# Kernel optimization log

Measured on AMD Instinct MI355X. Metric: run time of the kernel, lower is better.

## Reference

```python
import jax, jax.numpy as jnp
import numpy as np

# surrogate-gradient spike (multi-gaussian, standard DH-SNN act_fun_adp constants)
GAMMA, LENS, SCALE, HIGHT = 0.5, 0.5, 6.0, 0.15
B_J0, BETA_ADAPT, VTH = 1.6, 1.8, 1.0
IN_DIM, N1, N2, OUT_DIM, BRANCH = 76, 50, 100, 2, 4
BATCH, SEQ = 256, 1000

def _gauss(x, mu, sigma):
    return jnp.exp(-((x - mu) ** 2) / (2.0 * sigma ** 2)) / (jnp.sqrt(2.0 * jnp.pi) * sigma)

@jax.custom_vjp
def spike_fn(x):
    return (x > 0).astype(x.dtype)

def _spike_fwd(x):
    return spike_fn(x), x

def _spike_bwd(x, g):
    sg = (_gauss(x, 0.0, LENS) * (1.0 + HIGHT)
          - _gauss(x, LENS, SCALE * LENS) * HIGHT
          - _gauss(x, -LENS, SCALE * LENS) * HIGHT)
    return (g * sg * GAMMA,)

spike_fn.defvjp(_spike_fwd, _spike_bwd)

def branch_mask(in_dim, out_dim, branch):
    # each dendritic branch k sees contiguous chunk k of the (input|recurrent) vector
    isize = in_dim + out_dim
    seg = int(np.ceil(isize / branch))
    m = np.zeros((out_dim * branch, isize), np.float32)
    for k in range(branch):
        m[k::branch, k * seg:min((k + 1) * seg, isize)] = 1.0
    return jnp.asarray(m)

def setup_inputs():
    key = jax.random.key(0)
    ks = jax.random.split(key, 12)
    def lin(k, o, i):
        lim = 1.0 / np.sqrt(i)
        kw, kb = jax.random.split(k)
        return (jax.random.uniform(kw, (o, i), jnp.float32, -lim, lim),
                jax.random.uniform(kb, (o,), jnp.float32, -lim, lim))
    W1, b1 = lin(ks[0], N1 * BRANCH, IN_DIM + N1)
    W2, b2 = lin(ks[1], N2 * BRANCH, N1 + N2)
    Wx, bx = lin(ks[2], N2, 2 * N2)
    Wm, bm = lin(ks[3], N2, 2 * N2)
    Wa, ba = lin(ks[4], N2, 2 * N2)
    Wd = jax.random.normal(ks[5], (OUT_DIM, N2), jnp.float32) * np.sqrt(2.0 / (OUT_DIM + N2))
    bd = jnp.zeros((OUT_DIM,), jnp.float32)
    tau_m1 = jax.random.uniform(ks[6], (N1,), jnp.float32, 0.0, 4.0)
    tau_n1 = jax.random.uniform(ks[7], (N1, BRANCH), jnp.float32, 0.0, 4.0)
    tau_m2 = jax.random.uniform(ks[8], (N2,), jnp.float32, 0.0, 4.0)
    tau_n2 = jax.random.uniform(ks[9], (N2, BRANCH), jnp.float32, 0.0, 4.0)
    tau_md = jax.random.uniform(ks[10], (OUT_DIM,), jnp.float32, 0.0, 4.0)
    x = jax.random.normal(ks[11], (BATCH, SEQ, IN_DIM), jnp.float32)
    return dict(x=x, W1=W1, b1=b1, tau_m1=tau_m1, tau_n1=tau_n1,
                W2=W2, b2=b2, tau_m2=tau_m2, tau_n2=tau_n2,
                Wx=Wx, bx=bx, Wm=Wm, bm=bm, Wa=Wa, ba=ba,
                Wd=Wd, bd=bd, tau_md=tau_md)

def _denri_step(xt, mem, spk, d, W, b, tau_m, tau_n, n_out):
    # dendritic spiking neuron (spike_rnn_test_denri_wotanh_R)
    kin = jnp.concatenate([xt, spk], axis=1)                       # [B, in+out]
    beta = jax.nn.sigmoid(tau_n)                                   # [out, branch]
    proj = (kin @ W.T + b).reshape(-1, n_out, BRANCH)              # [B, out, branch]
    d = beta * d + (1.0 - beta) * proj
    alpha = jax.nn.sigmoid(tau_m)
    mem = mem * alpha + (1.0 - alpha) * d.sum(-1) - VTH * spk
    spk = spike_fn(mem - VTH)
    return mem, spk, d

def _liquid_step(xt, mem, spk, bth, Wx, bx, Wm, bm, Wa, ba):
    # liquid time-constant adaptive-threshold cell (SNN_rec_cell, is_rec=True)
    dx = jnp.concatenate([xt, spk], axis=1) @ Wx.T + bx
    tauM = jax.nn.sigmoid(jnp.concatenate([dx, mem], axis=1) @ Wm.T + bm)
    tauA = jax.nn.sigmoid(jnp.concatenate([dx, bth], axis=1) @ Wa.T + ba)
    bth = tauA * bth + (1.0 - tauA) * spk
    B = B_J0 + BETA_ADAPT * bth
    mem = mem * tauM + (1.0 - tauM) * dx - B * spk
    spk = spike_fn(mem - B)
    return mem, spk, bth

def reference(x, W1, b1, tau_m1, tau_n1, W2, b2, tau_m2, tau_n2,
              Wx, bx, Wm, bm, Wa, ba, Wd, bd, tau_md):
    Bsz = x.shape[0]
    W1m = W1 * branch_mask(IN_DIM, N1, BRANCH)
    W2m = W2 * branch_mask(N1, N2, BRANCH)
    alpha_d = jax.nn.sigmoid(tau_md)
    z = lambda *s: jnp.zeros(s, x.dtype)
    carry0 = (z(Bsz, N1), z(Bsz, N1), z(Bsz, N1, BRANCH),
              z(Bsz, N2), z(Bsz, N2), z(Bsz, N2, BRANCH),
              z(Bsz, N2), z(Bsz, N2), jnp.full((Bsz, N2), B_J0, x.dtype),
              z(Bsz, OUT_DIM))

    def step(carry, xt):
        m1, s1, d1, m2, s2, d2, lm, ls, lb, md = carry
        m1, s1, d1 = _denri_step(xt, m1, s1, d1, W1m, b1, tau_m1, tau_n1, N1)
        m2, s2, d2 = _denri_step(s1, m2, s2, d2, W2m, b2, tau_m2, tau_n2, N2)
        # original detaches the liquid hidden tuple every step
        lm, ls, lb = (jax.lax.stop_gradient(t) for t in (lm, ls, lb))
        lm, ls, lb = _liquid_step(s2, lm, ls, lb, Wx, bx, Wm, bm, Wa, ba)
        md = md * alpha_d + (1.0 - alpha_d) * (ls @ Wd.T + bd)    # readout integrator
        return (m1, s1, d1, m2, s2, d2, lm, ls, lb, md), md

    _, md_seq = jax.lax.scan(step, carry0, jnp.swapaxes(x, 0, 1))  # [T, B, OUT]
    return md_seq[1:].sum(axis=0)  # output only accumulated for i > 0
```

## Files before the change

kernel.cpp:

```cpp
#include <hip/hip_runtime.h>
#include <math.h>

#define SEQ 1000
#define IND 76
#define PIDX(i) ((((i)/25)*28) + ((i)%25))

__device__ __forceinline__ float sigf(float v) { return 1.0f / (1.0f + expf(-v)); }

__global__ __launch_bounds__(512) void dhsnn_fwd(
    const float* __restrict__ x,
    const float* __restrict__ W1, const float* __restrict__ b1,
    const float* __restrict__ tau_m1, const float* __restrict__ tau_n1,
    const float* __restrict__ W2, const float* __restrict__ b2,
    const float* __restrict__ tau_m2, const float* __restrict__ tau_n2,
    const float* __restrict__ Wxp, const float* __restrict__ bxp,
    const float* __restrict__ Wm, const float* __restrict__ bm,
    const float* __restrict__ Wa, const float* __restrict__ ba,
    const float* __restrict__ Wd, const float* __restrict__ bd,
    const float* __restrict__ tau_md,
    float* __restrict__ out)
{
    const int t   = (int)threadIdx.x;
    const int blk = (int)blockIdx.x;

    __shared__ __align__(16) float kin1P[128];
    __shared__ __align__(16) float kin2P[4][40];
    __shared__ __align__(16) float s1stage[56];
    __shared__ __align__(16) float dsum[400];
    __shared__ __align__(16) float dpart[8][100];
    __shared__ __align__(16) float spart[8][200];
    __shared__ __align__(16) float dxP[112];
    __shared__ __align__(16) float s2P[112];
    __shared__ __align__(16) float lsP[112];
    __shared__ __align__(16) float lmP[112];
    __shared__ __align__(16) float lbP[112];
    __shared__ __align__(16) float tauA_s[100];
    __shared__ __align__(16) float rpart[200];
    __shared__ __align__(16) float r2[8];

    for (int i = t; i < 128;  i += 512) kin1P[i] = 0.f;
    for (int i = t; i < 160;  i += 512) (&kin2P[0][0])[i] = 0.f;
    for (int i = t; i < 56;   i += 512) s1stage[i] = 0.f;
    for (int i = t; i < 400;  i += 512) dsum[i] = 0.f;
    for (int i = t; i < 800;  i += 512) (&dpart[0][0])[i] = 0.f;
    for (int i = t; i < 1600; i += 512) (&spart[0][0])[i] = 0.f;
    for (int i = t; i < 112;  i += 512) { dxP[i]=0.f; s2P[i]=0.f; lsP[i]=0.f; lmP[i]=0.f; lbP[i]=0.f; }
    for (int i = t; i < 100;  i += 512) tauA_s[i] = 0.f;
    for (int i = t; i < 200;  i += 512) rpart[i] = 0.f;
    for (int i = t; i < 8;    i += 512) r2[i] = 0.f;

    float wreg[188];
    float sc[10];
    float st[8];
    float mdr = 0.f, accr = 0.f;
    float4 xp0;
    #pragma unroll
    for (int i = 0; i < 10; ++i) sc[i] = 0.f;
    #pragma unroll
    for (int i = 0; i < 8; ++i)  st[i] = 0.f;

    if (t < 456) {
        const bool late = (t >= 256);
        const int  s    = late ? (t - 256) : t;
        if (s < 200) {
            const int g = s >> 2, c = s & 3;
            const int colbase = late ? (25 * c) : (100 + 25 * c);
            #pragma unroll
            for (int k = 0; k < 4; ++k) {
                const int row = 4 * g + k;
                const float* Wrow = (row < 100) ? (Wm + row * 200) : (Wa + (row - 100) * 200);
                #pragma unroll
                for (int u = 0; u < 25; ++u) wreg[k * 25 + u] = Wrow[colbase + u];
            }
            #pragma unroll
            for (int k = 0; k < 2; ++k) {
                const int row = 2 * g + k;
                #pragma unroll
                for (int u = 0; u < 25; ++u) wreg[100 + k * 25 + u] = Wxp[row * 200 + colbase + u];
            }
        }
        if (t < 400) {
            const int br = t & 3;
            #pragma unroll
            for (int cc = 0; cc < 38; ++cc) {
                const int gc = 38 * br + cc;
                wreg[150 + cc] = (gc < 150) ? W2[t * 150 + gc] : 0.f;
            }
            sc[0] = b2[t];
            sc[1] = sigf(tau_n2[t]);
        }
        if (t < 200) sc[5] = Wd[(t < 100 ? 0 : 100) + (t % 100)];
        if (t < 100) { sc[2] = sigf(tau_m2[t]); sc[3] = bxp[t]; sc[4] = bm[t]; st[3] = 1.6f; }
        else if (t < 200) sc[4] = ba[t - 100];
        if (t < 2) { sc[6] = sigf(tau_md[t]); sc[7] = bd[t]; }
    } else if (t < 506) {
        const int n = t - 456;
        #pragma unroll
        for (int k = 0; k < 4; ++k) {
            #pragma unroll
            for (int u = 0; u < 32; ++u) {
                const int gc = 32 * k + u;
                wreg[k * 32 + u] = (gc < 126) ? W1[(4 * n + k) * 126 + gc] : 0.f;
            }
            sc[k]     = b1[4 * n + k];
            sc[4 + k] = sigf(tau_n1[4 * n + k]);
        }
        sc[8] = sigf(tau_m1[n]);
    }

    auto l1_step = [&]() {
        float pr0 = sc[0], pr1 = sc[1], pr2 = sc[2], pr3 = sc[3];
        #pragma unroll
        for (int u4 = 0; u4 < 8; ++u4) {
            const float4 a0 = *reinterpret_cast<const float4*>(&kin1P[ 0 + 4 * u4]);
            const float4 a1 = *reinterpret_cast<const float4*>(&kin1P[32 + 4 * u4]);
            const float4 a2 = *reinterpret_cast<const float4*>(&kin1P[64 + 4 * u4]);
            const float4 a3 = *reinterpret_cast<const float4*>(&kin1P[96 + 4 * u4]);
            pr0 = fmaf(wreg[      4*u4+0], a0.x, pr0); pr0 = fmaf(wreg[      4*u4+1], a0.y, pr0);
            pr0 = fmaf(wreg[      4*u4+2], a0.z, pr0); pr0 = fmaf(wreg[      4*u4+3], a0.w, pr0);
            pr1 = fmaf(wreg[ 32 + 4*u4+0], a1.x, pr1); pr1 = fmaf(wreg[ 32 + 4*u4+1], a1.y, pr1);
            pr1 = fmaf(wreg[ 32 + 4*u4+2], a1.z, pr1); pr1 = fmaf(wreg[ 32 + 4*u4+3], a1.w, pr1);
            pr2 = fmaf(wreg[ 64 + 4*u4+0], a2.x, pr2); pr2 = fmaf(wreg[ 64 + 4*u4+1], a2.y, pr2);
            pr2 = fmaf(wreg[ 64 + 4*u4+2], a2.z, pr2); pr2 = fmaf(wreg[ 64 + 4*u4+3], a2.w, pr2);
            pr3 = fmaf(wreg[ 96 + 4*u4+0], a3.x, pr3); pr3 = fmaf(wreg[ 96 + 4*u4+1], a3.y, pr3);
            pr3 = fmaf(wreg[ 96 + 4*u4+2], a3.z, pr3); pr3 = fmaf(wreg[ 96 + 4*u4+3], a3.w, pr3);
        }
        const float d0 = sc[4] * st[0] + (1.f - sc[4]) * pr0;
        const float d1 = sc[5] * st[1] + (1.f - sc[5]) * pr1;
        const float d2 = sc[6] * st[2] + (1.f - sc[6]) * pr2;
        const float d3 = sc[7] * st[3] + (1.f - sc[7]) * pr3;
        st[0] = d0; st[1] = d1; st[2] = d2; st[3] = d3;
        const float sum = ((d0 + d1) + d2) + d3;
        st[4] = sc[8] * st[4] + (1.f - sc[8]) * sum - st[5];
        st[5] = (st[4] - 1.0f > 0.f) ? 1.f : 0.f;
        s1stage[t - 456] = st[5];
    };

    __syncthreads();
    if (t < 100) lbP[PIDX(t)] = 1.6f;
    if (t < 19) {
        const float4 v = *reinterpret_cast<const float4*>(x + (size_t)blk * SEQ * IND + 4 * t);
        *reinterpret_cast<float4*>(&kin1P[4 * t]) = v;
    }
    __syncthreads();
    if (t >= 456 && t < 506) l1_step();
    __syncthreads();
    if (t >= 128 && t < 178) {
        const int i2 = t - 128;
        const float v = s1stage[i2];
        kin1P[76 + i2] = v;
        const int w = i2 / 38;
        kin2P[w][i2 - 38 * w] = v;
    }
    if (t < 19) {
        const float4 v = *reinterpret_cast<const float4*>(x + ((size_t)blk * SEQ + 1) * IND + 4 * t);
        *reinterpret_cast<float4*>(&kin1P[4 * t]) = v;
    }
    __syncthreads();

    for (int j = 0; j < SEQ; ++j) {
        if (t >= 456) {
            if (t < 506 && j < SEQ - 1) l1_step();
        } else {
            if (t < 400) {
                const float* kw = kin2P[t & 3];
                float a0 = 0.f, a1 = 0.f, a2 = 0.f, a3 = 0.f;
                #pragma unroll
                for (int cc = 0; cc < 9; ++cc) {
                    const float4 av = *reinterpret_cast<const float4*>(kw + 4 * cc);
                    a0 = fmaf(wreg[150 + 4*cc + 0], av.x, a0);
                    a1 = fmaf(wreg[150 + 4*cc + 1], av.y, a1);
                    a2 = fmaf(wreg[150 + 4*cc + 2], av.z, a2);
                    a3 = fmaf(wreg[150 + 4*cc + 3], av.w, a3);
                }
                a0 = fmaf(wreg[186], kw[36], a0);
                a1 = fmaf(wreg[187], kw[37], a1);
                const float proj = sc[0] + ((a0 + a1) + (a2 + a3));
                st[0] = sc[1] * st[0] + (1.f - sc[1]) * proj;
                dsum[t] = st[0];
            }
            if (t < 200) {
                const int g = t >> 2, c = t & 3;
                {
                    const float* ap = ((g < 25) ? lmP : lbP) + 28 * c;
                    float e0=0.f, e1=0.f, e2=0.f, e3=0.f;
                    #pragma unroll
                    for (int u4 = 0; u4 < 6; ++u4) {
                        const float4 av = *reinterpret_cast<const float4*>(ap + 4 * u4);
                        e0 = fmaf(wreg[  0 + 4*u4+0], av.x, e0); e0 = fmaf(wreg[  0 + 4*u4+1], av.y, e0);
                        e0 = fmaf(wreg[  0 + 4*u4+2], av.z, e0); e0 = fmaf(wreg[  0 + 4*u4+3], av.w, e0);
                        e1 = fmaf(wreg[ 25 + 4*u4+0], av.x, e1); e1 = fmaf(wreg[ 25 + 4*u4+1], av.y, e1);
                        e1 = fmaf(wreg[ 25 + 4*u4+2], av.z, e1); e1 = fmaf(wreg[ 25 + 4*u4+3], av.w, e1);
                        e2 = fmaf(wreg[ 50 + 4*u4+0], av.x, e2); e2 = fmaf(wreg[ 50 + 4*u4+1], av.y, e2);
                        e2 = fmaf(wreg[ 50 + 4*u4+2], av.z, e2); e2 = fmaf(wreg[ 50 + 4*u4+3], av.w, e2);
                        e3 = fmaf(wreg[ 75 + 4*u4+0], av.x, e3); e3 = fmaf(wreg[ 75 + 4*u4+1], av.y, e3);
                        e3 = fmaf(wreg[ 75 + 4*u4+2], av.z, e3); e3 = fmaf(wreg[ 75 + 4*u4+3], av.w, e3);
                    }
                    const float al = ap[24];
                    e0 = fmaf(wreg[24], al, e0); e1 = fmaf(wreg[49], al, e1);
                    e2 = fmaf(wreg[74], al, e2); e3 = fmaf(wreg[99], al, e3);
                    spart[c][4*g+0] = e0; spart[c][4*g+1] = e1;
                    spart[c][4*g+2] = e2; spart[c][4*g+3] = e3;
                }
                {
                    const float* ap = lsP + 28 * c;
                    float f0 = 0.f, f1 = 0.f;
                    #pragma unroll
                    for (int u4 = 0; u4 < 6; ++u4) {
                        const float4 av = *reinterpret_cast<const float4*>(ap + 4 * u4);
                        f0 = fmaf(wreg[100 + 4*u4+0], av.x, f0); f0 = fmaf(wreg[100 + 4*u4+1], av.y, f0);
                        f0 = fmaf(wreg[100 + 4*u4+2], av.z, f0); f0 = fmaf(wreg[100 + 4*u4+3], av.w, f0);
                        f1 = fmaf(wreg[125 + 4*u4+0], av.x, f1); f1 = fmaf(wreg[125 + 4*u4+1], av.y, f1);
                        f1 = fmaf(wreg[125 + 4*u4+2], av.z, f1); f1 = fmaf(wreg[125 + 4*u4+3], av.w, f1);
                    }
                    const float al = ap[24];
                    f0 = fmaf(wreg[124], al, f0);
                    f1 = fmaf(wreg[149], al, f1);
                    dpart[c][2*g+0] = f0;
                    dpart[c][2*g+1] = f1;
                }
                rpart[t] = sc[5] * lsP[PIDX(t % 100)];
            } else if (t < 219) {
                if (j + 2 < SEQ)
                    xp0 = *reinterpret_cast<const float4*>(x + ((size_t)blk * SEQ + (j + 2)) * IND + 4 * (t - 200));
            }
        }
        __syncthreads();
        if (t < 100) {
            const float4 dv = *reinterpret_cast<const float4*>(&dsum[4 * t]);
            const float sum = ((dv.x + dv.y) + dv.z) + dv.w;
            st[1] = sc[2] * st[1] + (1.f - sc[2]) * sum - st[7];
            st[7] = (st[1] - 1.0f > 0.f) ? 1.f : 0.f;
            const int col = 50 + t, w = col / 38;
            kin2P[w][col - 38 * w] = st[7];
            s2P[PIDX(t)] = st[7];
        } else if (t >= 256 && t < 264) {
            const int rr = t - 256;
            float sV = 0.f;
            #pragma unroll
            for (int u = 0; u < 25; ++u) sV += rpart[25 * rr + u];
            r2[rr] = sV;
        }
        __syncthreads();
        if (t >= 256 && t < 456) {
            const int s = t - 256;
            const int g = s >> 2, c = s & 3;
            const float* ap = s2P + 28 * c;
            float f0 = 0.f, f1 = 0.f;
            #pragma unroll
            for (int u4 = 0; u4 < 6; ++u4) {
                const float4 av = *reinterpret_cast<const float4*>(ap + 4 * u4);
                f0 = fmaf(wreg[100 + 4*u4+0], av.x, f0); f0 = fmaf(wreg[100 + 4*u4+1], av.y, f0);
                f0 = fmaf(wreg[100 + 4*u4+2], av.z, f0); f0 = fmaf(wreg[100 + 4*u4+3], av.w, f0);
                f1 = fmaf(wreg[125 + 4*u4+0], av.x, f1); f1 = fmaf(wreg[125 + 4*u4+1], av.y, f1);
                f1 = fmaf(wreg[125 + 4*u4+2], av.z, f1); f1 = fmaf(wreg[125 + 4*u4+3], av.w, f1);
            }
            const float al = ap[24];
            f0 = fmaf(wreg[124], al, f0);
            f1 = fmaf(wreg[149], al, f1);
            dpart[4 + c][2*g+0] = f0;
            dpart[4 + c][2*g+1] = f1;
        } else if (t >= 200 && t < 219) {
            if (j + 2 < SEQ)
                *reinterpret_cast<float4*>(&kin1P[4 * (t - 200)]) = xp0;
        }
        __syncthreads();
        if (t < 100) {
            const float sV = (((dpart[4][t] + dpart[5][t]) + (dpart[6][t] + dpart[7][t]))
                            + ((dpart[0][t] + dpart[1][t]) + (dpart[2][t] + dpart[3][t]))) + sc[3];
            st[5] = sV;
            dxP[PIDX(t)] = sV;
        }
        if (t < 2 && j >= 1) {
            const float dot = ((r2[4*t+0] + r2[4*t+1]) + (r2[4*t+2] + r2[4*t+3])) + sc[7];
            mdr = sc[6] * mdr + (1.f - sc[6]) * dot;
            if (j >= 2) accr += mdr;
        }
        __syncthreads();
        if (t >= 256 && t < 456) {
            const int s = t - 256;
            const int g = s >> 2, c = s & 3;
            const float* ap = dxP + 28 * c;
            float e0=0.f, e1=0.f, e2=0.f, e3=0.f;
            #pragma unroll
            for (int u4 = 0; u4 < 6; ++u4) {
                const float4 av = *reinterpret_cast<const float4*>(ap + 4 * u4);
                e0 = fmaf(wreg[  0 + 4*u4+0], av.x, e0); e0 = fmaf(wreg[  0 + 4*u4+1], av.y, e0);
                e0 = fmaf(wreg[  0 + 4*u4+2], av.z, e0); e0 = fmaf(wreg[  0 + 4*u4+3], av.w, e0);
                e1 = fmaf(wreg[ 25 + 4*u4+0], av.x, e1); e1 = fmaf(wreg[ 25 + 4*u4+1], av.y, e1);
                e1 = fmaf(wreg[ 25 + 4*u4+2], av.z, e1); e1 = fmaf(wreg[ 25 + 4*u4+3], av.w, e1);
                e2 = fmaf(wreg[ 50 + 4*u4+0], av.x, e2); e2 = fmaf(wreg[ 50 + 4*u4+1], av.y, e2);
                e2 = fmaf(wreg[ 50 + 4*u4+2], av.z, e2); e2 = fmaf(wreg[ 50 + 4*u4+3], av.w, e2);
                e3 = fmaf(wreg[ 75 + 4*u4+0], av.x, e3); e3 = fmaf(wreg[ 75 + 4*u4+1], av.y, e3);
                e3 = fmaf(wreg[ 75 + 4*u4+2], av.z, e3); e3 = fmaf(wreg[ 75 + 4*u4+3], av.w, e3);
            }
            const float al = ap[24];
            e0 = fmaf(wreg[24], al, e0); e1 = fmaf(wreg[49], al, e1);
            e2 = fmaf(wreg[74], al, e2); e3 = fmaf(wreg[99], al, e3);
            spart[4 + c][4*g+0] = e0; spart[4 + c][4*g+1] = e1;
            spart[4 + c][4*g+2] = e2; spart[4 + c][4*g+3] = e3;
        }
        __syncthreads();
        if (t < 200) {
            const float sV = (((spart[4][t] + spart[5][t]) + (spart[6][t] + spart[7][t]))
                            + ((spart[0][t] + spart[1][t]) + (spart[2][t] + spart[3][t]))) + sc[4];
            const float tv = 1.f / (1.f + expf(-sV));
            if (t < 100) st[6] = tv;
            else tauA_s[t - 100] = tv;
        }
        __syncthreads();
        if (t < 100) {
            const float ta  = tauA_s[t];
            const float lbN = ta * st[3] + (1.f - ta) * st[4];
            const float Bv  = 1.6f + 1.8f * lbN;
            const float lmN = st[2] * st[6] + (1.f - st[6]) * st[5] - Bv * st[4];
            const float lsN = (lmN - Bv > 0.f) ? 1.f : 0.f;
            st[2] = lmN; st[3] = lbN; st[4] = lsN;
            lmP[PIDX(t)] = lmN; lbP[PIDX(t)] = lbN; lsP[PIDX(t)] = lsN;
        } else if (t >= 128 && t < 178) {
            const int i2 = t - 128;
            const float v = s1stage[i2];
            kin1P[76 + i2] = v;
            const int w = i2 / 38;
            kin2P[w][i2 - 38 * w] = v;
        }
        __syncthreads();
    }

    if (t < 200) rpart[t] = sc[5] * lsP[PIDX(t % 100)];
    __syncthreads();
    if (t >= 256 && t < 264) {
        const int rr = t - 256;
        float sV = 0.f;
        #pragma unroll
        for (int u = 0; u < 25; ++u) sV += rpart[25 * rr + u];
        r2[rr] = sV;
    }
    __syncthreads();
    if (t < 2) {
        const float dot = ((r2[4*t+0] + r2[4*t+1]) + (r2[4*t+2] + r2[4*t+3])) + sc[7];
        mdr = sc[6] * mdr + (1.f - sc[6]) * dot;
        accr += mdr;
        out[blk * 2 + t] = accr;
    }
}

extern "C" void kernel_launch(void* const* d_in, const int* in_sizes, int n_in,
                              void* d_out, int out_size, void* d_ws, size_t ws_size,
                              hipStream_t stream) {
    const float* x      = (const float*)d_in[0];
    const float* W1     = (const float*)d_in[1];
    const float* b1     = (const float*)d_in[2];
    const float* tau_m1 = (const float*)d_in[3];
    const float* tau_n1 = (const float*)d_in[4];
    const float* W2     = (const float*)d_in[5];
    const float* b2     = (const float*)d_in[6];
    const float* tau_m2 = (const float*)d_in[7];
    const float* tau_n2 = (const float*)d_in[8];
    const float* Wx     = (const float*)d_in[9];
    const float* bx     = (const float*)d_in[10];
    const float* bm     = (const float*)d_in[12];
    const float* Wm     = (const float*)d_in[11];
    const float* Wa     = (const float*)d_in[13];
    const float* ba     = (const float*)d_in[14];
    const float* Wd     = (const float*)d_in[15];
    const float* bd     = (const float*)d_in[16];
    const float* tau_md = (const float*)d_in[17];
    float* out = (float*)d_out;

    const int batch = in_sizes[0] / (SEQ * IND);
    dhsnn_fwd<<<batch, 512, 0, stream>>>(x, W1, b1, tau_m1, tau_n1,
                                         W2, b2, tau_m2, tau_n2,
                                         Wx, bx, Wm, bm, Wa, ba,
                                         Wd, bd, tau_md, out);
}
```

Baseline: 4.654 ms.

## Restructure per-step work split to cut barriers using wave shuffles

Reassigns the 400 layer-2 threads so each group of four lanes owns one neuron, computing dendritic sums and the liquid-layer matvecs over half or quarter slices and combining partial sums with intra-wave shuffles. This replaces shared-memory partial arrays (dsum, dpart, spart, tauA_s) and cuts the barriers per timestep from six to three. It also sets launch bounds to two blocks per CU. The cost is a larger per-thread register array, more redundant work per lane, and possible spilling under the tighter register budget.

```diff
diff --git a/kernel.cpp b/kernel.cpp
--- a/kernel.cpp
+++ b/kernel.cpp
@@ -3,11 +3,16 @@
 
 #define SEQ 1000
 #define IND 76
-#define PIDX(i) ((((i)/25)*28) + ((i)%25))
 
 __device__ __forceinline__ float sigf(float v) { return 1.0f / (1.0f + expf(-v)); }
 
-__global__ __launch_bounds__(512) void dhsnn_fwd(
+#define W2O 0
+#define SEO 38
+#define SLO 90
+#define XEO 142
+#define XLO 170
+
+__global__ __launch_bounds__(512, 2) void dhsnn_fwd(
     const float* __restrict__ x,
     const float* __restrict__ W1, const float* __restrict__ b1,
     const float* __restrict__ tau_m1, const float* __restrict__ tau_n1,
@@ -26,75 +31,72 @@
     __shared__ __align__(16) float kin1P[128];
     __shared__ __align__(16) float kin2P[4][40];
     __shared__ __align__(16) float s1stage[56];
-    __shared__ __align__(16) float dsum[400];
-    __shared__ __align__(16) float dpart[8][100];
-    __shared__ __align__(16) float spart[8][200];
-    __shared__ __align__(16) float dxP[112];
-    __shared__ __align__(16) float s2P[112];
-    __shared__ __align__(16) float lsP[112];
-    __shared__ __align__(16) float lmP[112];
-    __shared__ __align__(16) float lbP[112];
-    __shared__ __align__(16) float tauA_s[100];
+    __shared__ __align__(16) float s2P[104];
+    __shared__ __align__(16) float dxP[104];
+    __shared__ __align__(16) float lsP[104];
+    __shared__ __align__(16) float lmP[104];
+    __shared__ __align__(16) float lbP[104];
     __shared__ __align__(16) float rpart[200];
     __shared__ __align__(16) float r2[8];
 
-    for (int i = t; i < 128;  i += 512) kin1P[i] = 0.f;
-    for (int i = t; i < 160;  i += 512) (&kin2P[0][0])[i] = 0.f;
-    for (int i = t; i < 56;   i += 512) s1stage[i] = 0.f;
-    for (int i = t; i < 400;  i += 512) dsum[i] = 0.f;
-    for (int i = t; i < 800;  i += 512) (&dpart[0][0])[i] = 0.f;
-    for (int i = t; i < 1600; i += 512) (&spart[0][0])[i] = 0.f;
-    for (int i = t; i < 112;  i += 512) { dxP[i]=0.f; s2P[i]=0.f; lsP[i]=0.f; lmP[i]=0.f; lbP[i]=0.f; }
-    for (int i = t; i < 100;  i += 512) tauA_s[i] = 0.f;
-    for (int i = t; i < 200;  i += 512) rpart[i] = 0.f;
-    for (int i = t; i < 8;    i += 512) r2[i] = 0.f;
-
-    float wreg[188];
-    float sc[10];
-    float st[8];
+    for (int i = t; i < 128; i += 512) kin1P[i] = 0.f;
+    for (int i = t; i < 160; i += 512) (&kin2P[0][0])[i] = 0.f;
+    for (int i = t; i < 56;  i += 512) s1stage[i] = 0.f;
+    for (int i = t; i < 104; i += 512) { s2P[i]=0.f; dxP[i]=0.f; lsP[i]=0.f; lmP[i]=0.f; lbP[i]=0.f; }
+    for (int i = t; i < 200; i += 512) rpart[i] = 0.f;
+    for (int i = t; i < 8;   i += 512) r2[i] = 0.f;
+
+    const int q = t >> 2;
+    const int c = t & 3;
+    const int h = c & 1;
+    const int lbase = (t & 63) & ~3;
+
+    float wreg[198];
+    float sc[9];
+    float st[7];
+    float eAcc = 0.f, dAcc = 0.f;
     float mdr = 0.f, accr = 0.f;
     float4 xp0;
+    int doff = 0;
     #pragma unroll
-    for (int i = 0; i < 10; ++i) sc[i] = 0.f;
+    for (int i = 0; i < 9; ++i) sc[i] = 0.f;
     #pragma unroll
-    for (int i = 0; i < 8; ++i)  st[i] = 0.f;
-
-    if (t < 456) {
-        const bool late = (t >= 256);
-        const int  s    = late ? (t - 256) : t;
-        if (s < 200) {
-            const int g = s >> 2, c = s & 3;
-            const int colbase = late ? (25 * c) : (100 + 25 * c);
-            #pragma unroll
-            for (int k = 0; k < 4; ++k) {
-                const int row = 4 * g + k;
-                const float* Wrow = (row < 100) ? (Wm + row * 200) : (Wa + (row - 100) * 200);
-                #pragma unroll
-                for (int u = 0; u < 25; ++u) wreg[k * 25 + u] = Wrow[colbase + u];
-            }
-            #pragma unroll
-            for (int k = 0; k < 2; ++k) {
-                const int row = 2 * g + k;
-                #pragma unroll
-                for (int u = 0; u < 25; ++u) wreg[100 + k * 25 + u] = Wxp[row * 200 + colbase + u];
-            }
-        }
-        if (t < 400) {
-            const int br = t & 3;
-            #pragma unroll
-            for (int cc = 0; cc < 38; ++cc) {
-                const int gc = 38 * br + cc;
-                wreg[150 + cc] = (gc < 150) ? W2[t * 150 + gc] : 0.f;
-            }
-            sc[0] = b2[t];
-            sc[1] = sigf(tau_n2[t]);
-        }
-        if (t < 200) sc[5] = Wd[(t < 100 ? 0 : 100) + (t % 100)];
-        if (t < 100) { sc[2] = sigf(tau_m2[t]); sc[3] = bxp[t]; sc[4] = bm[t]; st[3] = 1.6f; }
-        else if (t < 200) sc[4] = ba[t - 100];
-        if (t < 2) { sc[6] = sigf(tau_md[t]); sc[7] = bd[t]; }
-    } else if (t < 506) {
-        const int n = t - 456;
+    for (int i = 0; i < 7; ++i) st[i] = 0.f;
+
+    if (t < 400) {
+        #pragma unroll
+        for (int cc = 0; cc < 38; ++cc) {
+            const int gc = 38 * c + cc;
+            wreg[W2O + cc] = (gc < 150) ? W2[t * 150 + gc] : 0.f;
+        }
+        sc[0] = b2[t];
+        sc[1] = sigf(tau_n2[t]);
+        const float* Wrow = (c < 2) ? (Wm + q * 200) : (Wa + q * 200);
+        const int eoff = h ? 52 : 0;
+        #pragma unroll
+        for (int u = 0; u < 52; ++u) {
+            const int col = eoff + u;
+            const bool ok = (col < 100);
+            wreg[SEO + u] = ok ? Wrow[100 + col] : 0.f;
+            wreg[SLO + u] = ok ? Wrow[col] : 0.f;
+        }
+        doff = (c == 0) ? 0 : (4 + 24 * c);
+        const int dcnt = (c == 0) ? 28 : 24;
+        #pragma unroll
+        for (int u = 0; u < 28; ++u) {
+            const int col = doff + u;
+            const bool ok = (u < dcnt);
+            wreg[XEO + u] = ok ? Wxp[q * 200 + 100 + col] : 0.f;
+            wreg[XLO + u] = ok ? Wxp[q * 200 + col] : 0.f;
+        }
+        if (c == 0) {
+            sc[2] = sigf(tau_m2[q]);
+            sc[3] = bm[q]; sc[4] = ba[q]; sc[5] = bxp[q];
+            st[4] = 1.6f;
+        }
+        if (t < 200) sc[6] = Wd[(t < 100 ? 0 : 100) + (t % 100)];
+    } else if (t >= 448 && t < 498) {
+        const int n = t - 448;
         #pragma unroll
         for (int k = 0; k < 4; ++k) {
             #pragma unroll
@@ -106,6 +108,9 @@
             sc[4 + k] = sigf(tau_n1[4 * n + k]);
         }
         sc[8] = sigf(tau_m1[n]);
+    } else if (t == 420 || t == 421) {
+        sc[0] = sigf(tau_md[t - 420]);
+        sc[1] = bd[t - 420];
     }
 
     auto l1_step = [&]() {
@@ -133,17 +138,17 @@
         const float sum = ((d0 + d1) + d2) + d3;
         st[4] = sc[8] * st[4] + (1.f - sc[8]) * sum - st[5];
         st[5] = (st[4] - 1.0f > 0.f) ? 1.f : 0.f;
-        s1stage[t - 456] = st[5];
+        s1stage[t - 448] = st[5];
     };
 
     __syncthreads();
-    if (t < 100) lbP[PIDX(t)] = 1.6f;
+    if (t < 100) lbP[t] = 1.6f;
     if (t < 19) {
         const float4 v = *reinterpret_cast<const float4*>(x + (size_t)blk * SEQ * IND + 4 * t);
         *reinterpret_cast<float4*>(&kin1P[4 * t]) = v;
     }
     __syncthreads();
-    if (t >= 456 && t < 506) l1_step();
+    if (t >= 448 && t < 498) l1_step();
     __syncthreads();
     if (t >= 128 && t < 178) {
         const int i2 = t - 128;
@@ -159,189 +164,161 @@
     __syncthreads();
 
     for (int j = 0; j < SEQ; ++j) {
-        if (t >= 456) {
-            if (t < 506 && j < SEQ - 1) l1_step();
-        } else {
-            if (t < 400) {
-                const float* kw = kin2P[t & 3];
+        if (t < 400) {
+            {
+                const float* kw = kin2P[c];
                 float a0 = 0.f, a1 = 0.f, a2 = 0.f, a3 = 0.f;
                 #pragma unroll
                 for (int cc = 0; cc < 9; ++cc) {
                     const float4 av = *reinterpret_cast<const float4*>(kw + 4 * cc);
-                    a0 = fmaf(wreg[150 + 4*cc + 0], av.x, a0);
-                    a1 = fmaf(wreg[150 + 4*cc + 1], av.y, a1);
-                    a2 = fmaf(wreg[150 + 4*cc + 2], av.z, a2);
-                    a3 = fmaf(wreg[150 + 4*cc + 3], av.w, a3);
+                    a0 = fmaf(wreg[W2O + 4*cc + 0], av.x, a0);
+                    a1 = fmaf(wreg[W2O + 4*cc + 1], av.y, a1);
+                    a2 = fmaf(wreg[W2O + 4*cc + 2], av.z, a2);
+                    a3 = fmaf(wreg[W2O + 4*cc + 3], av.w, a3);
                 }
-                a0 = fmaf(wreg[186], kw[36], a0);
-                a1 = fmaf(wreg[187], kw[37], a1);
+                a0 = fmaf(wreg[W2O + 36], kw[36], a0);
+                a1 = fmaf(wreg[W2O + 37], kw[37], a1);
                 const float proj = sc[0] + ((a0 + a1) + (a2 + a3));
                 st[0] = sc[1] * st[0] + (1.f - sc[1]) * proj;
-                dsum[t] = st[0];
-            }
-            if (t < 200) {
-                const int g = t >> 2, c = t & 3;
-                {
-                    const float* ap = ((g < 25) ? lmP : lbP) + 28 * c;
-                    float e0=0.f, e1=0.f, e2=0.f, e3=0.f;
-                    #pragma unroll
-                    for (int u4 = 0; u4 < 6; ++u4) {
-                        const float4 av = *reinterpret_cast<const float4*>(ap + 4 * u4);
-                        e0 = fmaf(wreg[  0 + 4*u4+0], av.x, e0); e0 = fmaf(wreg[  0 + 4*u4+1], av.y, e0);
-                        e0 = fmaf(wreg[  0 + 4*u4+2], av.z, e0); e0 = fmaf(wreg[  0 + 4*u4+3], av.w, e0);
-                        e1 = fmaf(wreg[ 25 + 4*u4+0], av.x, e1); e1 = fmaf(wreg[ 25 + 4*u4+1], av.y, e1);
-                        e1 = fmaf(wreg[ 25 + 4*u4+2], av.z, e1); e1 = fmaf(wreg[ 25 + 4*u4+3], av.w, e1);
-                        e2 = fmaf(wreg[ 50 + 4*u4+0], av.x, e2); e2 = fmaf(wreg[ 50 + 4*u4+1], av.y, e2);
-                        e2 = fmaf(wreg[ 50 + 4*u4+2], av.z, e2); e2 = fmaf(wreg[ 50 + 4*u4+3], av.w, e2);
-                        e3 = fmaf(wreg[ 75 + 4*u4+0], av.x, e3); e3 = fmaf(wreg[ 75 + 4*u4+1], av.y, e3);
-                        e3 = fmaf(wreg[ 75 + 4*u4+2], av.z, e3); e3 = fmaf(wreg[ 75 + 4*u4+3], av.w, e3);
-                    }
-                    const float al = ap[24];
-                    e0 = fmaf(wreg[24], al, e0); e1 = fmaf(wreg[49], al, e1);
-                    e2 = fmaf(wreg[74], al, e2); e3 = fmaf(wreg[99], al, e3);
-                    spart[c][4*g+0] = e0; spart[c][4*g+1] = e1;
-                    spart[c][4*g+2] = e2; spart[c][4*g+3] = e3;
+                const float dme = st[0];
+                const float dd1 = __shfl(dme, lbase + 1, 64);
+                const float dd2 = __shfl(dme, lbase + 2, 64);
+                const float dd3 = __shfl(dme, lbase + 3, 64);
+                if (c == 0) {
+                    const float sum = ((dme + dd1) + dd2) + dd3;
+                    st[1] = sc[2] * st[1] + (1.f - sc[2]) * sum - st[2];
+                    st[2] = (st[1] - 1.0f > 0.f) ? 1.f : 0.f;
+                    s2P[q] = st[2];
                 }
-                {
-                    const float* ap = lsP + 28 * c;
-                    float f0 = 0.f, f1 = 0.f;
-                    #pragma unroll
-                    for (int u4 = 0; u4 < 6; ++u4) {
-                        const float4 av = *reinterpret_cast<const float4*>(ap + 4 * u4);
-                        f0 = fmaf(wreg[100 + 4*u4+0], av.x, f0); f0 = fmaf(wreg[100 + 4*u4+1], av.y, f0);
-                        f0 = fmaf(wreg[100 + 4*u4+2], av.z, f0); f0 = fmaf(wreg[100 + 4*u4+3], av.w, f0);
-                        f1 = fmaf(wreg[125 + 4*u4+0], av.x, f1); f1 = fmaf(wreg[125 + 4*u4+1], av.y, f1);
-                        f1 = fmaf(wreg[125 + 4*u4+2], av.z, f1); f1 = fmaf(wreg[125 + 4*u4+3], av.w, f1);
-                    }
-                    const float al = ap[24];
-                    f0 = fmaf(wreg[124], al, f0);
-                    f1 = fmaf(wreg[149], al, f1);
-                    dpart[c][2*g+0] = f0;
-                    dpart[c][2*g+1] = f1;
+            }
+            {
+                const float* ap = ((c < 2) ? lmP : lbP) + (h ? 52 : 0);
+                float e0=0.f, e1=0.f, e2=0.f, e3=0.f;
+                #pragma unroll
+                for (int u4 = 0; u4 < 13; ++u4) {
+                    const float4 av = *reinterpret_cast<const float4*>(ap + 4 * u4);
+                    e0 = fmaf(wreg[SEO + 4*u4 + 0], av.x, e0);
+                    e1 = fmaf(wreg[SEO + 4*u4 + 1], av.y, e1);
+                    e2 = fmaf(wreg[SEO + 4*u4 + 2], av.z, e2);
+                    e3 = fmaf(wreg[SEO + 4*u4 + 3], av.w, e3);
                 }
-                rpart[t] = sc[5] * lsP[PIDX(t % 100)];
-            } else if (t < 219) {
-                if (j + 2 < SEQ)
-                    xp0 = *reinterpret_cast<const float4*>(x + ((size_t)blk * SEQ + (j + 2)) * IND + 4 * (t - 200));
-            }
+                eAcc = (e0 + e1) + (e2 + e3);
+            }
+            {
+                const float* ap = lsP + doff;
+                float f0=0.f, f1=0.f, f2=0.f, f3=0.f;
+                #pragma unroll
+                for (int u4 = 0; u4 < 7; ++u4) {
+                    const float4 av = *reinterpret_cast<const float4*>(ap + 4 * u4);
+                    f0 = fmaf(wreg[XEO + 4*u4 + 0], av.x, f0);
+                    f1 = fmaf(wreg[XEO + 4*u4 + 1], av.y, f1);
+                    f2 = fmaf(wreg[XEO + 4*u4 + 2], av.z, f2);
+                    f3 = fmaf(wreg[XEO + 4*u4 + 3], av.w, f3);
+                }
+                dAcc = (f0 + f1) + (f2 + f3);
+            }
+            if (t < 200) rpart[t] = sc[6] * lsP[t % 100];
+        } else if (t < 419) {
+            if (j + 2 < SEQ)
+                xp0 = *reinterpret_cast<const float4*>(x + ((size_t)blk * SEQ + (j + 2)) * IND + 4 * (t - 400));
+        } else if (t >= 448 && t < 498) {
+            if (j < SEQ - 1) l1_step();
         }
         __syncthreads();
-        if (t < 100) {
-            const float4 dv = *reinterpret_cast<const float4*>(&dsum[4 * t]);
-            const float sum = ((dv.x + dv.y) + dv.z) + dv.w;
-            st[1] = sc[2] * st[1] + (1.f - sc[2]) * sum - st[7];
-            st[7] = (st[1] - 1.0f > 0.f) ? 1.f : 0.f;
-            const int col = 50 + t, w = col / 38;
-            kin2P[w][col - 38 * w] = st[7];
-            s2P[PIDX(t)] = st[7];
-        } else if (t >= 256 && t < 264) {
-            const int rr = t - 256;
+        if (t < 400) {
+            const float* ap = s2P + doff;
+            float f0=0.f, f1=0.f, f2=0.f, f3=0.f;
+            #pragma unroll
+            for (int u4 = 0; u4 < 7; ++u4) {
+                const float4 av = *reinterpret_cast<const float4*>(ap + 4 * u4);
+                f0 = fmaf(wreg[XLO + 4*u4 + 0], av.x, f0);
+                f1 = fmaf(wreg[XLO + 4*u4 + 1], av.y, f1);
+                f2 = fmaf(wreg[XLO + 4*u4 + 2], av.z, f2);
+                f3 = fmaf(wreg[XLO + 4*u4 + 3], av.w, f3);
+            }
+            const float tot = ((f0 + f1) + (f2 + f3)) + dAcc;
+            const float t1 = __shfl(tot, lbase + 1, 64);
+            const float t2 = __shfl(tot, lbase + 2, 64);
+            const float t3 = __shfl(tot, lbase + 3, 64);
+            if (c == 0) {
+                const float dxv = ((tot + t1) + (t2 + t3)) + sc[5];
+                st[6] = dxv;
+                dxP[q] = dxv;
+                const int col = 50 + q;
+                const int w = (col >= 114) ? 3 : ((col >= 76) ? 2 : 1);
+                kin2P[w][col - 38 * w] = st[2];
+            }
+        } else if (t < 419) {
+            if (j + 2 < SEQ)
+                *reinterpret_cast<float4*>(&kin1P[4 * (t - 400)]) = xp0;
+        } else if (t >= 424 && t < 432) {
+            const int rr = t - 424;
             float sV = 0.f;
             #pragma unroll
             for (int u = 0; u < 25; ++u) sV += rpart[25 * rr + u];
             r2[rr] = sV;
         }
         __syncthreads();
-        if (t >= 256 && t < 456) {
-            const int s = t - 256;
-            const int g = s >> 2, c = s & 3;
-            const float* ap = s2P + 28 * c;
-            float f0 = 0.f, f1 = 0.f;
-            #pragma unroll
-            for (int u4 = 0; u4 < 6; ++u4) {
-                const float4 av = *reinterpret_cast<const float4*>(ap + 4 * u4);
-                f0 = fmaf(wreg[100 + 4*u4+0], av.x, f0); f0 = fmaf(wreg[100 + 4*u4+1], av.y, f0);
-                f0 = fmaf(wreg[100 + 4*u4+2], av.z, f0); f0 = fmaf(wreg[100 + 4*u4+3], av.w, f0);
-                f1 = fmaf(wreg[125 + 4*u4+0], av.x, f1); f1 = fmaf(wreg[125 + 4*u4+1], av.y, f1);
-                f1 = fmaf(wreg[125 + 4*u4+2], av.z, f1); f1 = fmaf(wreg[125 + 4*u4+3], av.w, f1);
-            }
-            const float al = ap[24];
-            f0 = fmaf(wreg[124], al, f0);
-            f1 = fmaf(wreg[149], al, f1);
-            dpart[4 + c][2*g+0] = f0;
-            dpart[4 + c][2*g+1] = f1;
-        } else if (t >= 200 && t < 219) {
-            if (j + 2 < SEQ)
-                *reinterpret_cast<float4*>(&kin1P[4 * (t - 200)]) = xp0;
-        }
-        __syncthreads();
-        if (t < 100) {
-            const float sV = (((dpart[4][t] + dpart[5][t]) + (dpart[6][t] + dpart[7][t]))
-                            + ((dpart[0][t] + dpart[1][t]) + (dpart[2][t] + dpart[3][t]))) + sc[3];
-            st[5] = sV;
-            dxP[PIDX(t)] = sV;
-        }
-        if (t < 2 && j >= 1) {
-            const float dot = ((r2[4*t+0] + r2[4*t+1]) + (r2[4*t+2] + r2[4*t+3])) + sc[7];
-            mdr = sc[6] * mdr + (1.f - sc[6]) * dot;
-            if (j >= 2) accr += mdr;
-        }
-        __syncthreads();
-        if (t >= 256 && t < 456) {
-            const int s = t - 256;
-            const int g = s >> 2, c = s & 3;
-            const float* ap = dxP + 28 * c;
+        if (t < 400) {
+            const float* ap = dxP + (h ? 52 : 0);
             float e0=0.f, e1=0.f, e2=0.f, e3=0.f;
             #pragma unroll
-            for (int u4 = 0; u4 < 6; ++u4) {
+            for (int u4 = 0; u4 < 13; ++u4) {
                 const float4 av = *reinterpret_cast<const float4*>(ap + 4 * u4);
-                e0 = fmaf(wreg[  0 + 4*u4+0], av.x, e0); e0 = fmaf(wreg[  0 + 4*u4+1], av.y, e0);
-                e0 = fmaf(wreg[  0 + 4*u4+2], av.z, e0); e0 = fmaf(wreg[  0 + 4*u4+3], av.w, e0);
-                e1 = fmaf(wreg[ 25 + 4*u4+0], av.x, e1); e1 = fmaf(wreg[ 25 + 4*u4+1], av.y, e1);
-                e1 = fmaf(wreg[ 25 + 4*u4+2], av.z, e1); e1 = fmaf(wreg[ 25 + 4*u4+3], av.w, e1);
-                e2 = fmaf(wreg[ 50 + 4*u4+0], av.x, e2); e2 = fmaf(wreg[ 50 + 4*u4+1], av.y, e2);
-                e2 = fmaf(wreg[ 50 + 4*u4+2], av.z, e2); e2 = fmaf(wreg[ 50 + 4*u4+3], av.w, e2);
-                e3 = fmaf(wreg[ 75 + 4*u4+0], av.x, e3); e3 = fmaf(wreg[ 75 + 4*u4+1], av.y, e3);
-                e3 = fmaf(wreg[ 75 + 4*u4+2], av.z, e3); e3 = fmaf(wreg[ 75 + 4*u4+3], av.w, e3);
-            }
-            const float al = ap[24];
-            e0 = fmaf(wreg[24], al, e0); e1 = fmaf(wreg[49], al, e1);
-            e2 = fmaf(wreg[74], al, e2); e3 = fmaf(wreg[99], al, e3);
-            spart[4 + c][4*g+0] = e0; spart[4 + c][4*g+1] = e1;
-            spart[4 + c][4*g+2] = e2; spart[4 + c][4*g+3] = e3;
-        }
-        __syncthreads();
-        if (t < 200) {
-            const float sV = (((spart[4][t] + spart[5][t]) + (spart[6][t] + spart[7][t]))
-                            + ((spart[0][t] + spart[1][t]) + (spart[2][t] + spart[3][t]))) + sc[4];
-            const float tv = 1.f / (1.f + expf(-sV));
-            if (t < 100) st[6] = tv;
-            else tauA_s[t - 100] = tv;
-        }
-        __syncthreads();
-        if (t < 100) {
-            const float ta  = tauA_s[t];
-            const float lbN = ta * st[3] + (1.f - ta) * st[4];
-            const float Bv  = 1.6f + 1.8f * lbN;
-            const float lmN = st[2] * st[6] + (1.f - st[6]) * st[5] - Bv * st[4];
-            const float lsN = (lmN - Bv > 0.f) ? 1.f : 0.f;
-            st[2] = lmN; st[3] = lbN; st[4] = lsN;
-            lmP[PIDX(t)] = lmN; lbP[PIDX(t)] = lbN; lsP[PIDX(t)] = lsN;
-        } else if (t >= 128 && t < 178) {
+                e0 = fmaf(wreg[SLO + 4*u4 + 0], av.x, e0);
+                e1 = fmaf(wreg[SLO + 4*u4 + 1], av.y, e1);
+                e2 = fmaf(wreg[SLO + 4*u4 + 2], av.z, e2);
+                e3 = fmaf(wreg[SLO + 4*u4 + 3], av.w, e3);
+            }
+            const float tot = ((e0 + e1) + (e2 + e3)) + eAcc;
+            const float t1 = __shfl(tot, lbase + 1, 64);
+            const float t2 = __shfl(tot, lbase + 2, 64);
+            const float t3 = __shfl(tot, lbase + 3, 64);
+            if (c == 0) {
+                const float preM = (tot + t1) + sc[3];
+                const float preA = (t2 + t3) + sc[4];
+                const float tm = sigf(preM);
+                const float ta = sigf(preA);
+                const float lbN = ta * st[4] + (1.f - ta) * st[5];
+                const float Bv  = 1.6f + 1.8f * lbN;
+                const float lmN = st[3] * tm + (1.f - tm) * st[6] - Bv * st[5];
+                const float lsN = (lmN - Bv > 0.f) ? 1.f : 0.f;
+                st[3] = lmN; st[4] = lbN; st[5] = lsN;
+                lmP[q] = lmN; lbP[q] = lbN; lsP[q] = lsN;
+            }
+        }
+        if (t >= 128 && t < 178) {
             const int i2 = t - 128;
             const float v = s1stage[i2];
             kin1P[76 + i2] = v;
             const int w = i2 / 38;
             kin2P[w][i2 - 38 * w] = v;
         }
+        if ((t == 420 || t == 421) && j >= 1) {
+            const int o = t - 420;
+            const float dot = ((r2[4*o] + r2[4*o+1]) + (r2[4*o+2] + r2[4*o+3])) + sc[1];
+            mdr = sc[0] * mdr + (1.f - sc[0]) * dot;
+            if (j >= 2) accr += mdr;
+        }
         __syncthreads();
     }
 
-    if (t < 200) rpart[t] = sc[5] * lsP[PIDX(t % 100)];
-    __syncthreads();
-    if (t >= 256 && t < 264) {
-        const int rr = t - 256;
+    if (t < 200) rpart[t] = sc[6] * lsP[t % 100];
+    __syncthreads();
+    if (t >= 424 && t < 432) {
+        const int rr = t - 424;
         float sV = 0.f;
         #pragma unroll
         for (int u = 0; u < 25; ++u) sV += rpart[25 * rr + u];
         r2[rr] = sV;
     }
     __syncthreads();
-    if (t < 2) {
-        const float dot = ((r2[4*t+0] + r2[4*t+1]) + (r2[4*t+2] + r2[4*t+3])) + sc[7];
-        mdr = sc[6] * mdr + (1.f - sc[6]) * dot;
+    if (t == 420 || t == 421) {
+        const int o = t - 420;
+        const float dot = ((r2[4*o] + r2[4*o+1]) + (r2[4*o+2] + r2[4*o+3])) + sc[1];
+        mdr = sc[0] * mdr + (1.f - sc[0]) * dot;
         accr += mdr;
-        out[blk * 2 + t] = accr;
+        out[blk * 2 + o] = accr;
     }
 }
 
@@ -359,8 +336,8 @@
     const float* tau_n2 = (const float*)d_in[8];
     const float* Wx     = (const float*)d_in[9];
     const float* bx     = (const float*)d_in[10];
+    const float* Wm     = (const float*)d_in[11];
     const float* bm     = (const float*)d_in[12];
-    const float* Wm     = (const float*)d_in[11];
     const float* Wa     = (const float*)d_in[13];
     const float* ba     = (const float*)d_in[14];
     const float* Wd     = (const float*)d_in[15];
```

After: 15.94 ms. 242% more time.
